# Optimization experiments

Hardware: AMD Instinct MI355X
Metric: run time of the kernel (lower is better)

Reference implementation:

```python
import jax, jax.numpy as jnp
import numpy as np
import math

B, S, D, H = 2, 2048, 1024, 16
DK = D // H


def setup_inputs() -> dict:
    key = jax.random.key(0)
    ks = jax.random.split(key, 12)
    std = 1.0 / math.sqrt(D)
    inp = {
        "q": jax.random.normal(ks[0], (B, S, D), jnp.float32),
        "k": jax.random.normal(ks[1], (B, S, D), jnp.float32),
        "v": jax.random.normal(ks[2], (B, S, D), jnp.float32),
        # causal mask, broadcast over batch and heads
        "mask": jnp.tril(jnp.ones((S, S), jnp.int32))[None, None, :, :],
        "wq": jax.random.normal(ks[3], (D, D), jnp.float32) * std,
        "bq": jax.random.normal(ks[4], (D,), jnp.float32) * std,
        "wk": jax.random.normal(ks[5], (D, D), jnp.float32) * std,
        "bk": jax.random.normal(ks[6], (D,), jnp.float32) * std,
        "wv": jax.random.normal(ks[7], (D, D), jnp.float32) * std,
        "bv": jax.random.normal(ks[8], (D,), jnp.float32) * std,
        "wo": jax.random.normal(ks[9], (D, D), jnp.float32) * std,
        "bo": jax.random.normal(ks[10], (D,), jnp.float32) * std,
    }
    return inp


def _split_heads(x):
    # [B,S,D] -> [B,H,S,DK]
    b, s, _ = x.shape
    return x.reshape(b, s, H, DK).transpose(0, 2, 1, 3)


def reference(q, k, v, mask, wq, bq, wk, bk, wv, bv, wo, bo):
    # nn.Linear: y = x @ W^T + b
    query = _split_heads(q @ wq.T + bq)
    key_h = _split_heads(k @ wk.T + bk)
    value = _split_heads(v @ wv.T + bv)

    scale = 1.0 / math.sqrt(DK)
    scores = jnp.einsum("bhqd,bhkd->bhqk", query, key_h) * scale  # [B,H,S,S]
    scores = jnp.where(mask == 0, jnp.float32(-1e9), scores)
    attn = jax.nn.softmax(scores, axis=-1)  # dropout p=0.0 -> identity

    x = jnp.einsum("bhqk,bhkd->bhqd", attn, value)  # [B,H,S,DK]
    x = x.transpose(0, 2, 1, 3).reshape(q.shape[0], -1, H * DK)  # [B,S,D]
    return x @ wo.T + bo
```

## Files before the change

kernel.cpp:

```cpp
#include <hip/hip_runtime.h>

#define B_SZ    2
#define S_LEN   2048
#define D_MODEL 1024
#define H_NUM   16
#define DK_H    64
#define M_ROWS  (B_SZ * S_LEN)

typedef __attribute__((ext_vector_type(8))) short  short8;
typedef __attribute__((ext_vector_type(4))) short  short4v;
typedef __attribute__((ext_vector_type(4))) float  floatx4;

__device__ __forceinline__ short f2b(float f) {
    union { float f; unsigned u; } x; x.f = f;
    unsigned u = x.u + 0x7fffu + ((x.u >> 16) & 1u);
    return (short)(u >> 16);
}

typedef __attribute__((address_space(1))) const unsigned int gu32;
typedef __attribute__((address_space(3))) unsigned int       lu32;
__device__ __forceinline__ void gload_lds16(const short* g, short* l) {
    __builtin_amdgcn_global_load_lds((gu32*)g, (lu32*)l, 16, 0, 0);
}

#define QSCALE 0.18033688011112042f
#define SM_SHIFT 12.0f

__global__ void cvt_all_kernel(const float* __restrict__ xq, const float* __restrict__ xk,
                               const float* __restrict__ xv, const float* __restrict__ wq,
                               const float* __restrict__ wk, const float* __restrict__ wv,
                               const float* __restrict__ wo,
                               short* __restrict__ oxq, short* __restrict__ oxk,
                               short* __restrict__ oxv, short* __restrict__ owq,
                               short* __restrict__ owk, short* __restrict__ owv,
                               short* __restrict__ owo)
{
    const int y = blockIdx.y;
    const float* in;
    short* out;
    switch (y) {
        case 0: in = xq; out = oxq; break;
        case 1: in = xk; out = oxk; break;
        case 2: in = xv; out = oxv; break;
        case 3: in = wq; out = owq; break;
        case 4: in = wk; out = owk; break;
        case 5: in = wv; out = owv; break;
        default: in = wo; out = owo; break;
    }
    const int npass = (y < 3) ? 4 : 1;
    int base = blockIdx.x * 1024 + threadIdx.x * 4;
    for (int p = 0; p < npass; ++p) {
        int i = base + p * 1048576;
        float4 v = *(const float4*)(in + i);
        short4v r;
        r[0] = f2b(v.x); r[1] = f2b(v.y); r[2] = f2b(v.z); r[3] = f2b(v.w);
        *(short4v*)(out + i) = r;
    }
}

__global__ __launch_bounds__(256)
void gemm_qkv_kernel(const short* __restrict__ xq, const short* __restrict__ xk,
                     const short* __restrict__ xv,
                     const short* __restrict__ wq, const short* __restrict__ wk,
                     const short* __restrict__ wv,
                     const float* __restrict__ bq, const float* __restrict__ bk,
                     const float* __restrict__ bv,
                     short* __restrict__ Qp, short* __restrict__ Kp, short* __restrict__ Vt)
{
    __shared__ short sa[128 * 32];
    __shared__ short sb[128 * 32];

    const int which = blockIdx.y >> 3;
    const short* A    = (which == 0) ? xq : (which == 1) ? xk : xv;
    const short* W    = (which == 0) ? wq : (which == 1) ? wk : wv;
    const float* bias = (which == 0) ? bq : (which == 1) ? bk : bv;
    const float scale = (which == 0) ? QSCALE : 1.0f;

    const int nb = (blockIdx.y & 7) * 128;
    const int m0 = blockIdx.x * 128;
    const int t = threadIdx.x, wave = t >> 6, lane = t & 63;
    const int quad = lane >> 4, l16 = lane & 15;
    const int wm = (wave & 1) * 64, wn = (wave >> 1) * 64;

    const int r0 = t >> 2, cs = t & 3;
    const int c0 = cs ^ ((r0 >> 1) & 3);
    const short* Ab0 = A + (size_t)(m0 + r0) * D_MODEL + c0 * 8;
    const short* Ab1 = Ab0 + (size_t)64 * D_MODEL;
    const short* Bb0 = W + (size_t)(nb + r0) * D_MODEL + c0 * 8;
    const short* Bb1 = Bb0 + (size_t)64 * D_MODEL;
    short* sa0 = sa + t * 8;  short* sa1 = sa + 2048 + t * 8;
    short* sb0 = sb + t * 8;  short* sb1 = sb + 2048 + t * 8;

    int a_off[4], b_off[4];
#pragma unroll
    for (int i = 0; i < 4; ++i) {
        int ar = wm + i * 16 + l16;
        a_off[i] = ar * 32 + ((quad ^ ((ar >> 1) & 3)) * 8);
        int br = wn + i * 16 + l16;
        b_off[i] = br * 32 + ((quad ^ ((br >> 1) & 3)) * 8);
    }

    floatx4 acc[4][4] = {};
    for (int k0 = 0; k0 < D_MODEL; k0 += 32) {
        __syncthreads();
        gload_lds16(Ab0 + k0, sa0);
        gload_lds16(Ab1 + k0, sa1);
        gload_lds16(Bb0 + k0, sb0);
        gload_lds16(Bb1 + k0, sb1);
        __syncthreads();
        short8 af[4], bf[4];
#pragma unroll
        for (int i = 0; i < 4; ++i) af[i] = *(const short8*)(sa + a_off[i]);
#pragma unroll
        for (int i = 0; i < 4; ++i) bf[i] = *(const short8*)(sb + b_off[i]);
#pragma unroll
        for (int mt = 0; mt < 4; ++mt)
#pragma unroll
            for (int nt = 0; nt < 4; ++nt)
                acc[mt][nt] = __builtin_amdgcn_mfma_f32_16x16x32_bf16(af[mt], bf[nt], acc[mt][nt], 0, 0, 0);
    }

#pragma unroll
    for (int nt = 0; nt < 4; ++nt) {
        int ncol = nb + wn + nt * 16 + l16;
        int h = ncol >> 6, dk = ncol & 63;
        float bv_ = bias[ncol];
#pragma unroll
        for (int mt = 0; mt < 4; ++mt) {
            int mrow0 = m0 + wm + mt * 16 + quad * 4;
            int bb = mrow0 >> 11, s0 = mrow0 & (S_LEN - 1);
            if (which < 2) {
                short* Out = (which == 0) ? Qp : Kp;
#pragma unroll
                for (int r = 0; r < 4; ++r) {
                    float v = (acc[mt][nt][r] + bv_) * scale;
                    Out[(((size_t)bb * H_NUM + h) * S_LEN + (s0 + r)) * DK_H + dk] = f2b(v);
                }
            } else {
                int Sb = s0 & ~63, sb0_ = s0 & 63;
                size_t rowbase = (((size_t)bb * H_NUM + h) * DK_H + dk) * S_LEN + Sb;
#pragma unroll
                for (int r = 0; r < 4; ++r) {
                    int cc = sb0_ + r;
                    Vt[rowbase + ((cc & 15) * 4 + (cc >> 4))] = f2b(acc[mt][nt][r] + bv_);
                }
            }
        }
    }
}

__global__ __launch_bounds__(512, 4)
void attn_kernel(const short* __restrict__ Qp, const short* __restrict__ Kp,
                 const short* __restrict__ Vt, short* __restrict__ Xa)
{
    __shared__ short kbuf[2][64 * 64];
    __shared__ short vbuf[2][64 * 64];
    __shared__ short pl[8][16 * 72];

    const int lin = (int)(blockIdx.x + 16 * blockIdx.y);
    const int bh = lin & 31;
    const int j8 = (lin >> 5) & 7;
    const int tile = (lin >> 8) ? (15 - j8) : j8;

    const int t = threadIdx.x, wave = t >> 6, lane = t & 63;
    const int quad = lane >> 4, l16 = lane & 15;

    const short* Qb  = Qp + (size_t)bh * S_LEN * DK_H;
    const short* Kb  = Kp + (size_t)bh * S_LEN * DK_H;
    const short* Vtb = Vt + (size_t)bh * DK_H * S_LEN;

    const int q0 = tile * 128 + wave * 16;
    const int my_ktimax = 2 * tile + (wave >> 2);
    const int ktb = 2 * tile + 1;

    const int r0 = t >> 3, cs = t & 7;
    const int c0 = cs ^ (r0 & 7);
    const short* Kg = Kb + r0 * DK_H + c0 * 8;
    const short* Vg = Vtb + (size_t)r0 * S_LEN + c0 * 8;
    short* kl0 = &kbuf[0][t * 8]; short* kl1 = &kbuf[1][t * 8];
    short* vl0 = &vbuf[0][t * 8]; short* vl1 = &vbuf[1][t * 8];

    short8 qf[2];
#pragma unroll
    for (int ks = 0; ks < 2; ++ks)
        qf[ks] = *(const short8*)(Qb + (size_t)(q0 + l16) * DK_H + ks * 32 + quad * 8);

    short8 bl = {};
    if (l16 == 0) {
#pragma unroll
        for (int j = 0; j < 8; ++j) bl[j] = (short)0x3F80;
    }

    int fo[4][2];
#pragma unroll
    for (int nt = 0; nt < 4; ++nt)
#pragma unroll
        for (int ks = 0; ks < 2; ++ks) {
            int row = nt * 16 + l16;
            fo[nt][ks] = row * 64 + (((ks * 4 + quad) ^ (l16 & 7)) * 8);
        }

    floatx4 o[4] = {};
    floatx4 ol = {};
    short* plw = &pl[wave][0];
    const int qg = q0 + quad * 4;

    gload_lds16(Kg, kl0);
    gload_lds16(Vg, vl0);
    __syncthreads();

    for (int kti = 0; kti <= ktb; ++kti) {
        const short* kb = (kti & 1) ? &kbuf[1][0] : &kbuf[0][0];
        const short* vb = (kti & 1) ? &vbuf[1][0] : &vbuf[0][0];
        const int kbase = kti * 64;

        if (kti < ktb) {
            gload_lds16(Kg + (size_t)(kbase + 64) * DK_H, (kti & 1) ? kl0 : kl1);
            gload_lds16(Vg + (kbase + 64),                (kti & 1) ? vl0 : vl1);
        }

        if (kti <= my_ktimax) {
            short8 bkf[4][2];
#pragma unroll
            for (int nt = 0; nt < 4; ++nt)
#pragma unroll
                for (int ks = 0; ks < 2; ++ks)
                    bkf[nt][ks] = *(const short8*)(kb + fo[nt][ks]);

            floatx4 sc[4] = {};
#pragma unroll
            for (int nt = 0; nt < 4; ++nt)
#pragma unroll
                for (int ks = 0; ks < 2; ++ks)
                    sc[nt] = __builtin_amdgcn_mfma_f32_16x16x32_bf16(qf[ks], bkf[nt][ks], sc[nt], 0, 0, 0);

            if (kti == my_ktimax) {
#pragma unroll
                for (int nt = 0; nt < 4; ++nt) {
                    int key = kbase + nt * 16 + l16;
#pragma unroll
                    for (int r = 0; r < 4; ++r)
                        if (key > qg + r) sc[nt][r] = -1e30f;
                }
            }

#pragma unroll
            for (int r = 0; r < 4; ++r) {
                union { float f; unsigned u; } a0, a1, a2, a3;
                a0.f = exp2f(sc[0][r] - SM_SHIFT);
                a1.f = exp2f(sc[1][r] - SM_SHIFT);
                a2.f = exp2f(sc[2][r] - SM_SHIFT);
                a3.f = exp2f(sc[3][r] - SM_SHIFT);
                uint2 d;
                d.x = (a1.u & 0xffff0000u) | (a0.u >> 16);
                d.y = (a3.u & 0xffff0000u) | (a2.u >> 16);
                *(uint2*)(plw + (quad * 4 + r) * 72 + l16 * 4) = d;
            }

            short8 ap0 = *(const short8*)(plw + l16 * 72 + quad * 8);
            short8 ap1 = *(const short8*)(plw + l16 * 72 + 32 + quad * 8);

            short8 bvf[4][2];
#pragma unroll
            for (int nt = 0; nt < 4; ++nt)
#pragma unroll
                for (int ks = 0; ks < 2; ++ks)
                    bvf[nt][ks] = *(const short8*)(vb + fo[nt][ks]);

#pragma unroll
            for (int nt = 0; nt < 4; ++nt) {
                o[nt] = __builtin_amdgcn_mfma_f32_16x16x32_bf16(ap0, bvf[nt][0], o[nt], 0, 0, 0);
                o[nt] = __builtin_amdgcn_mfma_f32_16x16x32_bf16(ap1, bvf[nt][1], o[nt], 0, 0, 0);
            }
            ol = __builtin_amdgcn_mfma_f32_16x16x32_bf16(ap0, bl, ol, 0, 0, 0);
            ol = __builtin_amdgcn_mfma_f32_16x16x32_bf16(ap1, bl, ol, 0, 0, 0);
        }

        __syncthreads();
    }

    const int b_ = bh >> 4, h = bh & 15;
#pragma unroll
    for (int r = 0; r < 4; ++r) {
        float lsum = __shfl(ol[r], (lane & 48));
        float rinv = 1.0f / lsum;
        int srow = qg + r;
#pragma unroll
        for (int nt = 0; nt < 4; ++nt) {
            int col = h * 64 + nt * 16 + l16;
            Xa[((size_t)b_ * S_LEN + srow) * D_MODEL + col] = f2b(o[nt][r] * rinv);
        }
    }
}

__global__ __launch_bounds__(256)
void gemm_out_kernel(const short* __restrict__ A, const short* __restrict__ W,
                     const float* __restrict__ bias, float* __restrict__ out)
{
    __shared__ short sa[128 * 32];
    __shared__ short sb[128 * 32];

    const int nb = blockIdx.y * 128;
    const int m0 = blockIdx.x * 128;
    const int t = threadIdx.x, wave = t >> 6, lane = t & 63;
    const int quad = lane >> 4, l16 = lane & 15;
    const int wm = (wave & 1) * 64, wn = (wave >> 1) * 64;

    const int r0 = t >> 2, cs = t & 3;
    const int c0 = cs ^ ((r0 >> 1) & 3);
    const short* Ab0 = A + (size_t)(m0 + r0) * D_MODEL + c0 * 8;
    const short* Ab1 = Ab0 + (size_t)64 * D_MODEL;
    const short* Bb0 = W + (size_t)(nb + r0) * D_MODEL + c0 * 8;
    const short* Bb1 = Bb0 + (size_t)64 * D_MODEL;
    short* sa0 = sa + t * 8;  short* sa1 = sa + 2048 + t * 8;
    short* sb0 = sb + t * 8;  short* sb1 = sb + 2048 + t * 8;

    int a_off[4], b_off[4];
#pragma unroll
    for (int i = 0; i < 4; ++i) {
        int ar = wm + i * 16 + l16;
        a_off[i] = ar * 32 + ((quad ^ ((ar >> 1) & 3)) * 8);
        int br = wn + i * 16 + l16;
        b_off[i] = br * 32 + ((quad ^ ((br >> 1) & 3)) * 8);
    }

    floatx4 acc[4][4] = {};
    for (int k0 = 0; k0 < D_MODEL; k0 += 32) {
        __syncthreads();
        gload_lds16(Ab0 + k0, sa0);
        gload_lds16(Ab1 + k0, sa1);
        gload_lds16(Bb0 + k0, sb0);
        gload_lds16(Bb1 + k0, sb1);
        __syncthreads();
        short8 af[4], bf[4];
#pragma unroll
        for (int i = 0; i < 4; ++i) af[i] = *(const short8*)(sa + a_off[i]);
#pragma unroll
        for (int i = 0; i < 4; ++i) bf[i] = *(const short8*)(sb + b_off[i]);
#pragma unroll
        for (int mt = 0; mt < 4; ++mt)
#pragma unroll
            for (int nt = 0; nt < 4; ++nt)
                acc[mt][nt] = __builtin_amdgcn_mfma_f32_16x16x32_bf16(af[mt], bf[nt], acc[mt][nt], 0, 0, 0);
    }

#pragma unroll
    for (int nt = 0; nt < 4; ++nt) {
        int ncol = nb + wn + nt * 16 + l16;
        float bv_ = bias[ncol];
#pragma unroll
        for (int mt = 0; mt < 4; ++mt) {
            int mrow0 = m0 + wm + mt * 16 + quad * 4;
#pragma unroll
            for (int r = 0; r < 4; ++r)
                out[(size_t)(mrow0 + r) * D_MODEL + ncol] = acc[mt][nt][r] + bv_;
        }
    }
}

extern "C" void kernel_launch(void* const* d_in, const int* in_sizes, int n_in,
                              void* d_out, int out_size, void* d_ws, size_t ws_size,
                              hipStream_t stream)
{
    (void)in_sizes; (void)n_in; (void)out_size; (void)ws_size;
    const float* q  = (const float*)d_in[0];
    const float* k  = (const float*)d_in[1];
    const float* v  = (const float*)d_in[2];
    const float* wq = (const float*)d_in[4];
    const float* bq = (const float*)d_in[5];
    const float* wk = (const float*)d_in[6];
    const float* bk = (const float*)d_in[7];
    const float* wv = (const float*)d_in[8];
    const float* bv = (const float*)d_in[9];
    const float* wo = (const float*)d_in[10];
    const float* bo = (const float*)d_in[11];
    float* out = (float*)d_out;

    const size_t XE = (size_t)M_ROWS * D_MODEL;
    const size_t WE = (size_t)D_MODEL * D_MODEL;
    short* ws_  = (short*)d_ws;
    short* xq_b = ws_;
    short* xk_b = xq_b + XE;
    short* xv_b = xk_b + XE;
    short* wq_b = xv_b + XE;
    short* wk_b = wq_b + WE;
    short* wv_b = wk_b + WE;
    short* wo_b = wv_b + WE;
    short* Qp   = wo_b + WE;
    short* Kp   = Qp + XE;
    short* Vt   = Kp + XE;
    short* Xa   = xq_b;

    dim3 blk(256);
    cvt_all_kernel<<<dim3(1024, 7), blk, 0, stream>>>(
        q, k, v, wq, wk, wv, wo, xq_b, xk_b, xv_b, wq_b, wk_b, wv_b, wo_b);

    gemm_qkv_kernel<<<dim3(M_ROWS / 128, 24), blk, 0, stream>>>(
        xq_b, xk_b, xv_b, wq_b, wk_b, wv_b, bq, bk, bv, Qp, Kp, Vt);

    attn_kernel<<<dim3(16, B_SZ * H_NUM), dim3(512), 0, stream>>>(Qp, Kp, Vt, Xa);

    gemm_out_kernel<<<dim3(M_ROWS / 128, D_MODEL / 128), blk, 0, stream>>>(Xa, wo_b, bo, out);
}
```

Measured before the change: 228.4 us.

## Rewrite QKV GEMM with 256x256 tiles and ping-pong pipelined LDS staging

```diff
diff --git a/kernel.cpp b/kernel.cpp
--- a/kernel.cpp
+++ b/kernel.cpp
@@ -25,6 +25,11 @@
 
 #define QSCALE 0.18033688011112042f
 #define SM_SHIFT 12.0f
+
+#define MFMA __builtin_amdgcn_mfma_f32_16x16x32_bf16
+#define BAR() __builtin_amdgcn_s_barrier()
+#define WAITV(n) do { asm volatile("s_waitcnt vmcnt(" #n ")" ::: "memory"); \
+                      __builtin_amdgcn_sched_barrier(0); } while (0)
 
 __global__ void cvt_all_kernel(const float* __restrict__ xq, const float* __restrict__ xk,
                                const float* __restrict__ xv, const float* __restrict__ wq,
@@ -58,7 +63,7 @@
     }
 }
 
-__global__ __launch_bounds__(256)
+__global__ __launch_bounds__(512, 2)
 void gemm_qkv_kernel(const short* __restrict__ xq, const short* __restrict__ xk,
                      const short* __restrict__ xv,
                      const short* __restrict__ wq, const short* __restrict__ wk,
@@ -67,86 +72,146 @@
                      const float* __restrict__ bv,
                      short* __restrict__ Qp, short* __restrict__ Kp, short* __restrict__ Vt)
 {
-    __shared__ short sa[128 * 32];
-    __shared__ short sb[128 * 32];
-
-    const int which = blockIdx.y >> 3;
+    extern __shared__ short lds[];
+
+    const int which = blockIdx.y >> 2;
     const short* A    = (which == 0) ? xq : (which == 1) ? xk : xv;
     const short* W    = (which == 0) ? wq : (which == 1) ? wk : wv;
     const float* bias = (which == 0) ? bq : (which == 1) ? bk : bv;
     const float scale = (which == 0) ? QSCALE : 1.0f;
 
-    const int nb = (blockIdx.y & 7) * 128;
-    const int m0 = blockIdx.x * 128;
+    const int nb = (blockIdx.y & 3) * 256;
+    const int m0 = blockIdx.x * 256;
     const int t = threadIdx.x, wave = t >> 6, lane = t & 63;
     const int quad = lane >> 4, l16 = lane & 15;
-    const int wm = (wave & 1) * 64, wn = (wave >> 1) * 64;
-
-    const int r0 = t >> 2, cs = t & 3;
-    const int c0 = cs ^ ((r0 >> 1) & 3);
-    const short* Ab0 = A + (size_t)(m0 + r0) * D_MODEL + c0 * 8;
-    const short* Ab1 = Ab0 + (size_t)64 * D_MODEL;
-    const short* Bb0 = W + (size_t)(nb + r0) * D_MODEL + c0 * 8;
-    const short* Bb1 = Bb0 + (size_t)64 * D_MODEL;
-    short* sa0 = sa + t * 8;  short* sa1 = sa + 2048 + t * 8;
-    short* sb0 = sb + t * 8;  short* sb1 = sb + 2048 + t * 8;
-
-    int a_off[4], b_off[4];
-#pragma unroll
-    for (int i = 0; i < 4; ++i) {
-        int ar = wm + i * 16 + l16;
-        a_off[i] = ar * 32 + ((quad ^ ((ar >> 1) & 3)) * 8);
-        int br = wn + i * 16 + l16;
-        b_off[i] = br * 32 + ((quad ^ ((br >> 1) & 3)) * 8);
-    }
-
-    floatx4 acc[4][4] = {};
-    for (int k0 = 0; k0 < D_MODEL; k0 += 32) {
-        __syncthreads();
-        gload_lds16(Ab0 + k0, sa0);
-        gload_lds16(Ab1 + k0, sa1);
-        gload_lds16(Bb0 + k0, sb0);
-        gload_lds16(Bb1 + k0, sb1);
-        __syncthreads();
-        short8 af[4], bf[4];
-#pragma unroll
-        for (int i = 0; i < 4; ++i) af[i] = *(const short8*)(sa + a_off[i]);
-#pragma unroll
-        for (int i = 0; i < 4; ++i) bf[i] = *(const short8*)(sb + b_off[i]);
-#pragma unroll
-        for (int mt = 0; mt < 4; ++mt)
-#pragma unroll
-            for (int nt = 0; nt < 4; ++nt)
-                acc[mt][nt] = __builtin_amdgcn_mfma_f32_16x16x32_bf16(af[mt], bf[nt], acc[mt][nt], 0, 0, 0);
-    }
-
-#pragma unroll
-    for (int nt = 0; nt < 4; ++nt) {
-        int ncol = nb + wn + nt * 16 + l16;
-        int h = ncol >> 6, dk = ncol & 63;
-        float bv_ = bias[ncol];
-#pragma unroll
-        for (int mt = 0; mt < 4; ++mt) {
-            int mrow0 = m0 + wm + mt * 16 + quad * 4;
-            int bb = mrow0 >> 11, s0 = mrow0 & (S_LEN - 1);
+    const int wr = wave >> 2, wc = wave & 3;
+
+    const int rs = t >> 3;
+    const int cl = (t & 7) ^ (rs & 7);
+    const short* Ag = A + (size_t)(m0 + rs) * D_MODEL + cl * 8;
+    const short* Wg = W + (size_t)(nb + rs) * D_MODEL + cl * 8;
+    short* sA = lds + t * 8;
+    short* sB = lds + 32768 + t * 8;
+
+#define STAGE_A(kt, h) do { const int _p = (kt) & 1;                                   \
+    gload_lds16(Ag + (size_t)((h) * 128) * D_MODEL + (kt) * 64,                        \
+                sA + _p * 16384 + (h) * 8192);                                         \
+    gload_lds16(Ag + (size_t)((h) * 128 + 64) * D_MODEL + (kt) * 64,                   \
+                sA + _p * 16384 + (h) * 8192 + 4096); } while (0)
+#define STAGE_B(kt, h) do { const int _p = (kt) & 1;                                   \
+    gload_lds16(Wg + (size_t)((h) * 128) * D_MODEL + (kt) * 64,                        \
+                sB + _p * 16384 + (h) * 8192);                                         \
+    gload_lds16(Wg + (size_t)((h) * 128 + 64) * D_MODEL + (kt) * 64,                   \
+                sB + _p * 16384 + (h) * 8192 + 4096); } while (0)
+
+    const short* aBase = lds + wr * 8192 + l16 * 64;
+    const short* bBase = lds + 32768 + wc * 4096 + l16 * 64;
+    const int ck0 = ((quad)     ^ (l16 & 7)) * 8;
+    const int ck1 = ((quad + 4) ^ (l16 & 7)) * 8;
+
+    short8 af[4][2], bf[4][2];
+    floatx4 acc[8][4] = {};
+
+#define LOAD_A(p, mh) do { _Pragma("unroll")                                           \
+    for (int mf = 0; mf < 4; ++mf) {                                                   \
+        af[mf][0] = *(const short8*)(aBase + (p) * 16384 + ((mh) * 4 + mf) * 1024 + ck0); \
+        af[mf][1] = *(const short8*)(aBase + (p) * 16384 + ((mh) * 4 + mf) * 1024 + ck1); \
+    } } while (0)
+#define LOAD_B2(p, nh) do { _Pragma("unroll")                                          \
+    for (int nf = 0; nf < 2; ++nf) {                                                   \
+        bf[(nh) * 2 + nf][0] = *(const short8*)(bBase + (p) * 16384 + ((nh) * 2 + nf) * 1024 + ck0); \
+        bf[(nh) * 2 + nf][1] = *(const short8*)(bBase + (p) * 16384 + ((nh) * 2 + nf) * 1024 + ck1); \
+    } } while (0)
+#define QUAD_MFMA(mh, nh) do {                                                         \
+    __builtin_amdgcn_s_setprio(1);                                                     \
+    _Pragma("unroll")                                                                  \
+    for (int mf = 0; mf < 4; ++mf) {                                                   \
+        _Pragma("unroll")                                                              \
+        for (int nf = 0; nf < 2; ++nf) {                                               \
+            acc[(mh)*4+mf][(nh)*2+nf] = MFMA(af[mf][0], bf[(nh)*2+nf][0], acc[(mh)*4+mf][(nh)*2+nf], 0, 0, 0); \
+            acc[(mh)*4+mf][(nh)*2+nf] = MFMA(af[mf][1], bf[(nh)*2+nf][1], acc[(mh)*4+mf][(nh)*2+nf], 0, 0, 0); \
+        }                                                                              \
+    }                                                                                  \
+    __builtin_amdgcn_s_setprio(0);                                                     \
+} while (0)
+
+    STAGE_A(0, 0);
+    STAGE_B(0, 0);
+    STAGE_B(0, 1);
+    STAGE_A(0, 1);
+    STAGE_A(1, 0);
+    WAITV(0);
+    BAR();
+
+#pragma unroll 1
+    for (int i = 0; i < 8; ++i) {
+        const int t1 = 2 * i + 1;
+        const int t2 = (2 * i + 2) & 15;
+        const int t3 = (2 * i + 3) & 15;
+
+        LOAD_A(0, 0); LOAD_B2(0, 0);
+        STAGE_B(t1, 0);
+        BAR(); QUAD_MFMA(0, 0); BAR();
+
+        LOAD_B2(0, 1);
+        STAGE_B(t1, 1);
+        BAR(); QUAD_MFMA(0, 1); WAITV(6); BAR();
+
+        LOAD_A(0, 1);
+        STAGE_A(t1, 1);
+        BAR(); QUAD_MFMA(1, 0); BAR();
+
+        STAGE_A(t2, 0);
+        BAR(); QUAD_MFMA(1, 1); WAITV(4); BAR();
+
+        LOAD_A(1, 0); LOAD_B2(1, 0);
+        STAGE_B(t2, 0);
+        BAR(); QUAD_MFMA(0, 0); BAR();
+
+        LOAD_B2(1, 1);
+        STAGE_B(t2, 1);
+        BAR(); QUAD_MFMA(0, 1); WAITV(6); BAR();
+
+        LOAD_A(1, 1);
+        STAGE_A(t2, 1);
+        BAR(); QUAD_MFMA(1, 0); BAR();
+
+        STAGE_A(t3, 0);
+        BAR(); QUAD_MFMA(1, 1); WAITV(4); BAR();
+    }
+
+#pragma unroll
+    for (int nf = 0; nf < 4; ++nf) {
+        const int ncol = nb + wc * 64 + nf * 16 + l16;
+        const int h = ncol >> 6, dk = ncol & 63;
+        const float bv_ = bias[ncol];
+#pragma unroll
+        for (int mf = 0; mf < 8; ++mf) {
+            const int mrow0 = m0 + wr * 128 + mf * 16 + quad * 4;
+            const int bb = mrow0 >> 11, s0 = mrow0 & (S_LEN - 1);
             if (which < 2) {
                 short* Out = (which == 0) ? Qp : Kp;
 #pragma unroll
                 for (int r = 0; r < 4; ++r) {
-                    float v = (acc[mt][nt][r] + bv_) * scale;
+                    float v = (acc[mf][nf][r] + bv_) * scale;
                     Out[(((size_t)bb * H_NUM + h) * S_LEN + (s0 + r)) * DK_H + dk] = f2b(v);
                 }
             } else {
-                int Sb = s0 & ~63, sb0_ = s0 & 63;
+                const int Sb = s0 & ~63, sb0_ = s0 & 63;
                 size_t rowbase = (((size_t)bb * H_NUM + h) * DK_H + dk) * S_LEN + Sb;
 #pragma unroll
                 for (int r = 0; r < 4; ++r) {
                     int cc = sb0_ + r;
-                    Vt[rowbase + ((cc & 15) * 4 + (cc >> 4))] = f2b(acc[mt][nt][r] + bv_);
+                    Vt[rowbase + ((cc & 15) * 4 + (cc >> 4))] = f2b(acc[mf][nf][r] + bv_);
                 }
             }
         }
     }
+#undef STAGE_A
+#undef STAGE_B
+#undef LOAD_A
+#undef LOAD_B2
+#undef QUAD_MFMA
 }
 
 __global__ __launch_bounds__(512, 4)
@@ -395,7 +460,7 @@
     cvt_all_kernel<<<dim3(1024, 7), blk, 0, stream>>>(
         q, k, v, wq, wk, wv, wo, xq_b, xk_b, xv_b, wq_b, wk_b, wv_b, wo_b);
 
-    gemm_qkv_kernel<<<dim3(M_ROWS / 128, 24), blk, 0, stream>>>(
+    gemm_qkv_kernel<<<dim3(M_ROWS / 256, 12), dim3(512), 131072, stream>>>(
         xq_b, xk_b, xv_b, wq_b, wk_b, wv_b, bq, bk, bv, Qp, Kp, Vt);
 
     attn_kernel<<<dim3(16, B_SZ * H_NUM), dim3(512), 0, stream>>>(Qp, Kp, Vt, Xa);
```

Result: slower. 240.3 us (+5.2%).

## Pre-tile weights into MFMA fragment layout and load B directly to registers

Applied to the files above, without the earlier changes.

```diff
diff --git a/kernel.cpp b/kernel.cpp
--- a/kernel.cpp
+++ b/kernel.cpp
@@ -47,18 +47,26 @@
         case 5: in = wv; out = owv; break;
         default: in = wo; out = owo; break;
     }
-    const int npass = (y < 3) ? 4 : 1;
     int base = blockIdx.x * 1024 + threadIdx.x * 4;
-    for (int p = 0; p < npass; ++p) {
-        int i = base + p * 1048576;
+    if (y < 3) {
+        for (int p = 0; p < 4; ++p) {
+            int i = base + p * 1048576;
+            float4 v = *(const float4*)(in + i);
+            short4v r;
+            r[0] = f2b(v.x); r[1] = f2b(v.y); r[2] = f2b(v.z); r[3] = f2b(v.w);
+            *(short4v*)(out + i) = r;
+        }
+    } else {
+        int i = base;
+        int n = i >> 10, k = i & 1023;
         float4 v = *(const float4*)(in + i);
         short4v r;
         r[0] = f2b(v.x); r[1] = f2b(v.y); r[2] = f2b(v.z); r[3] = f2b(v.w);
-        *(short4v*)(out + i) = r;
-    }
-}
-
-__global__ __launch_bounds__(256)
+        *(short4v*)(out + (((n >> 4) * 128 + (k >> 3)) * 128 + (n & 15) * 8 + (k & 4))) = r;
+    }
+}
+
+__global__ __launch_bounds__(256, 2)
 void gemm_qkv_kernel(const short* __restrict__ xq, const short* __restrict__ xk,
                      const short* __restrict__ xv,
                      const short* __restrict__ wq, const short* __restrict__ wk,
@@ -68,7 +76,6 @@
                      short* __restrict__ Qp, short* __restrict__ Kp, short* __restrict__ Vt)
 {
     __shared__ short sa[128 * 32];
-    __shared__ short sb[128 * 32];
 
     const int which = blockIdx.y >> 3;
     const short* A    = (which == 0) ? xq : (which == 1) ? xk : xv;
@@ -86,39 +93,53 @@
     const int c0 = cs ^ ((r0 >> 1) & 3);
     const short* Ab0 = A + (size_t)(m0 + r0) * D_MODEL + c0 * 8;
     const short* Ab1 = Ab0 + (size_t)64 * D_MODEL;
-    const short* Bb0 = W + (size_t)(nb + r0) * D_MODEL + c0 * 8;
-    const short* Bb1 = Bb0 + (size_t)64 * D_MODEL;
     short* sa0 = sa + t * 8;  short* sa1 = sa + 2048 + t * 8;
-    short* sb0 = sb + t * 8;  short* sb1 = sb + 2048 + t * 8;
-
-    int a_off[4], b_off[4];
+
+    int a_off[4];
 #pragma unroll
     for (int i = 0; i < 4; ++i) {
         int ar = wm + i * 16 + l16;
         a_off[i] = ar * 32 + ((quad ^ ((ar >> 1) & 3)) * 8);
-        int br = wn + i * 16 + l16;
-        b_off[i] = br * 32 + ((quad ^ ((br >> 1) & 3)) * 8);
-    }
+    }
+
+    const short* Wt = W + ((size_t)((nb + wn) >> 4) * 128 + quad) * 128 + l16 * 8;
+
+#define LOADB(dst, k0) do { _Pragma("unroll")                                  \
+    for (int nt_ = 0; nt_ < 4; ++nt_)                                          \
+        dst[nt_] = *(const short8*)(Wt + nt_ * 16384 + (k0) * 16); } while (0)
+
+    short8 bfA[4], bfB[4];
+    LOADB(bfA, 0);
 
     floatx4 acc[4][4] = {};
-    for (int k0 = 0; k0 < D_MODEL; k0 += 32) {
+#pragma unroll 1
+    for (int k0 = 0; k0 < D_MODEL; k0 += 64) {
         __syncthreads();
         gload_lds16(Ab0 + k0, sa0);
         gload_lds16(Ab1 + k0, sa1);
-        gload_lds16(Bb0 + k0, sb0);
-        gload_lds16(Bb1 + k0, sb1);
-        __syncthreads();
-        short8 af[4], bf[4];
-#pragma unroll
-        for (int i = 0; i < 4; ++i) af[i] = *(const short8*)(sa + a_off[i]);
-#pragma unroll
-        for (int i = 0; i < 4; ++i) bf[i] = *(const short8*)(sb + b_off[i]);
-#pragma unroll
-        for (int mt = 0; mt < 4; ++mt)
+        __syncthreads();
+        LOADB(bfB, k0 + 32);
+#pragma unroll
+        for (int mt = 0; mt < 4; ++mt) {
+            short8 af = *(const short8*)(sa + a_off[mt]);
 #pragma unroll
             for (int nt = 0; nt < 4; ++nt)
-                acc[mt][nt] = __builtin_amdgcn_mfma_f32_16x16x32_bf16(af[mt], bf[nt], acc[mt][nt], 0, 0, 0);
-    }
+                acc[mt][nt] = __builtin_amdgcn_mfma_f32_16x16x32_bf16(af, bfA[nt], acc[mt][nt], 0, 0, 0);
+        }
+        __syncthreads();
+        gload_lds16(Ab0 + k0 + 32, sa0);
+        gload_lds16(Ab1 + k0 + 32, sa1);
+        __syncthreads();
+        if (k0 + 64 < D_MODEL) LOADB(bfA, k0 + 64);
+#pragma unroll
+        for (int mt = 0; mt < 4; ++mt) {
+            short8 af = *(const short8*)(sa + a_off[mt]);
+#pragma unroll
+            for (int nt = 0; nt < 4; ++nt)
+                acc[mt][nt] = __builtin_amdgcn_mfma_f32_16x16x32_bf16(af, bfB[nt], acc[mt][nt], 0, 0, 0);
+        }
+    }
+#undef LOADB
 
 #pragma unroll
     for (int nt = 0; nt < 4; ++nt) {
@@ -293,59 +314,72 @@
     }
 }
 
-__global__ __launch_bounds__(256)
+__global__ __launch_bounds__(256, 2)
 void gemm_out_kernel(const short* __restrict__ A, const short* __restrict__ W,
                      const float* __restrict__ bias, float* __restrict__ out)
 {
     __shared__ short sa[128 * 32];
-    __shared__ short sb[128 * 32];
-
-    const int nb = blockIdx.y * 128;
+
+    const int nb = blockIdx.y * 64;
     const int m0 = blockIdx.x * 128;
     const int t = threadIdx.x, wave = t >> 6, lane = t & 63;
     const int quad = lane >> 4, l16 = lane & 15;
-    const int wm = (wave & 1) * 64, wn = (wave >> 1) * 64;
+    const int wm = (wave & 1) * 64, wn = (wave >> 1) * 32;
 
     const int r0 = t >> 2, cs = t & 3;
     const int c0 = cs ^ ((r0 >> 1) & 3);
     const short* Ab0 = A + (size_t)(m0 + r0) * D_MODEL + c0 * 8;
     const short* Ab1 = Ab0 + (size_t)64 * D_MODEL;
-    const short* Bb0 = W + (size_t)(nb + r0) * D_MODEL + c0 * 8;
-    const short* Bb1 = Bb0 + (size_t)64 * D_MODEL;
     short* sa0 = sa + t * 8;  short* sa1 = sa + 2048 + t * 8;
-    short* sb0 = sb + t * 8;  short* sb1 = sb + 2048 + t * 8;
-
-    int a_off[4], b_off[4];
+
+    int a_off[4];
 #pragma unroll
     for (int i = 0; i < 4; ++i) {
         int ar = wm + i * 16 + l16;
         a_off[i] = ar * 32 + ((quad ^ ((ar >> 1) & 3)) * 8);
-        int br = wn + i * 16 + l16;
-        b_off[i] = br * 32 + ((quad ^ ((br >> 1) & 3)) * 8);
-    }
-
-    floatx4 acc[4][4] = {};
-    for (int k0 = 0; k0 < D_MODEL; k0 += 32) {
+    }
+
+    const short* Wt = W + ((size_t)((nb + wn) >> 4) * 128 + quad) * 128 + l16 * 8;
+
+#define LOADB2(dst, k0) do { _Pragma("unroll")                                 \
+    for (int nt_ = 0; nt_ < 2; ++nt_)                                          \
+        dst[nt_] = *(const short8*)(Wt + nt_ * 16384 + (k0) * 16); } while (0)
+
+    short8 bfA[2], bfB[2];
+    LOADB2(bfA, 0);
+
+    floatx4 acc[4][2] = {};
+#pragma unroll 1
+    for (int k0 = 0; k0 < D_MODEL; k0 += 64) {
         __syncthreads();
         gload_lds16(Ab0 + k0, sa0);
         gload_lds16(Ab1 + k0, sa1);
-        gload_lds16(Bb0 + k0, sb0);
-        gload_lds16(Bb1 + k0, sb1);
-        __syncthreads();
-        short8 af[4], bf[4];
-#pragma unroll
-        for (int i = 0; i < 4; ++i) af[i] = *(const short8*)(sa + a_off[i]);
-#pragma unroll
-        for (int i = 0; i < 4; ++i) bf[i] = *(const short8*)(sb + b_off[i]);
-#pragma unroll
-        for (int mt = 0; mt < 4; ++mt)
-#pragma unroll
-            for (int nt = 0; nt < 4; ++nt)
-                acc[mt][nt] = __builtin_amdgcn_mfma_f32_16x16x32_bf16(af[mt], bf[nt], acc[mt][nt], 0, 0, 0);
-    }
-
-#pragma unroll
-    for (int nt = 0; nt < 4; ++nt) {
+        __syncthreads();
+        LOADB2(bfB, k0 + 32);
+#pragma unroll
+        for (int mt = 0; mt < 4; ++mt) {
+            short8 af = *(const short8*)(sa + a_off[mt]);
+#pragma unroll
+            for (int nt = 0; nt < 2; ++nt)
+                acc[mt][nt] = __builtin_amdgcn_mfma_f32_16x16x32_bf16(af, bfA[nt], acc[mt][nt], 0, 0, 0);
+        }
+        __syncthreads();
+        gload_lds16(Ab0 + k0 + 32, sa0);
+        gload_lds16(Ab1 + k0 + 32, sa1);
+        __syncthreads();
+        if (k0 + 64 < D_MODEL) LOADB2(bfA, k0 + 64);
+#pragma unroll
+        for (int mt = 0; mt < 4; ++mt) {
+            short8 af = *(const short8*)(sa + a_off[mt]);
+#pragma unroll
+            for (int nt = 0; nt < 2; ++nt)
+                acc[mt][nt] = __builtin_amdgcn_mfma_f32_16x16x32_bf16(af, bfB[nt], acc[mt][nt], 0, 0, 0);
+        }
+    }
+#undef LOADB2
+
+#pragma unroll
+    for (int nt = 0; nt < 2; ++nt) {
         int ncol = nb + wn + nt * 16 + l16;
         float bv_ = bias[ncol];
 #pragma unroll
@@ -400,5 +434,5 @@
 
     attn_kernel<<<dim3(16, B_SZ * H_NUM), dim3(512), 0, stream>>>(Qp, Kp, Vt, Xa);
 
-    gemm_out_kernel<<<dim3(M_ROWS / 128, D_MODEL / 128), blk, 0, stream>>>(Xa, wo_b, bo, out);
-}
+    gemm_out_kernel<<<dim3(M_ROWS / 128, D_MODEL / 64), blk, 0, stream>>>(Xa, wo_b, bo, out);
+}
```

Result: no change. 232.1 us (+1.6%).
